# Performance work log

Measured on AMD Instinct MI355X. Metric: run time of the kernel, lower is better.

## Reference

```python
import jax, jax.numpy as jnp
import numpy as np

N, D, H = 4096, 4096, 8          # total tokens, model dim (=hidden), heads
DH = D // H                      # head dim = 512
NEG = jnp.float32(-1e9)


def _make_num_rels():
    rng = np.random.default_rng(0)
    lens = rng.integers(96, 161, size=31)
    last = N - int(lens.sum())
    assert last > 0
    return np.concatenate([lens, [last]]).astype(np.int64)


def setup_inputs() -> dict:
    key = jax.random.key(0)
    ks = jax.random.split(key, 9)
    s = 0.02
    inp = {
        "prod_rep": jax.random.normal(ks[0], (N, D), dtype=jnp.float32),
        "num_rels": jnp.asarray(_make_num_rels()),
        # torch Linear weights stored transposed: [in, out]
        "Wq": jax.random.normal(ks[1], (D, D), dtype=jnp.float32) * s,
        "bq": jnp.zeros((D,), dtype=jnp.float32),
        "Wk": jax.random.normal(ks[2], (D, D), dtype=jnp.float32) * s,
        "bk": jnp.zeros((D,), dtype=jnp.float32),
        "Wv": jax.random.normal(ks[3], (D, D), dtype=jnp.float32) * s,
        "bv": jnp.zeros((D,), dtype=jnp.float32),
        "Wfc": jax.random.normal(ks[4], (D, D), dtype=jnp.float32) * s,
        "bfc": jnp.zeros((D,), dtype=jnp.float32),
    }
    return inp


def reference(prod_rep, num_rels, Wq, bq, Wk, bk, Wv, bv, Wfc, bfc):
    n = prod_rep.shape[0]
    # segment id per token (tokens are laid out contiguously per segment)
    cum = jnp.cumsum(num_rels)
    seg = jnp.searchsorted(cum, jnp.arange(n), side="right")  # [N]

    # fused QKV projections over all tokens at once
    q = (prod_rep @ Wq + bq).reshape(n, H, DH)
    k = (prod_rep @ Wk + bk).reshape(n, H, DH)
    v = (prod_rep @ Wv + bv).reshape(n, H, DH)

    # block-diagonal attention: tokens only attend within their own segment
    scores = jnp.einsum("nhd,mhd->hnm", q, k) / jnp.sqrt(jnp.float32(DH))
    mask = seg[:, None] == seg[None, :]                        # [N, N]
    scores = jnp.where(mask[None, :, :], scores, NEG)
    probs = jax.nn.softmax(scores, axis=-1)                    # [H, N, N]
    context = jnp.einsum("hnm,mhd->nhd", probs, v).reshape(n, D)

    res1 = context + prod_rep
    res2 = res1 + (res1 @ Wfc + bfc)
    return res2
```

## Files before the change

kernel.cpp:

```cpp
#include <hip/hip_runtime.h>
#include <hip/hip_bf16.h>
#include <cstdint>

typedef __bf16 bf16;
typedef __attribute__((ext_vector_type(4))) __bf16 bf16x4;
typedef __attribute__((ext_vector_type(8))) __bf16 bf16x8;
typedef __attribute__((ext_vector_type(4))) float f32x4;

#define AS1 __attribute__((address_space(1)))
#define AS3 __attribute__((address_space(3)))

__device__ __forceinline__ unsigned short f2bf(float x) {
    union { __bf16 b; unsigned short u; } c;
    c.b = (__bf16)x;
    return c.u;
}

__device__ __forceinline__ void gld_lds16(const void* g, void* lds_wave_base) {
#if __has_builtin(__builtin_amdgcn_global_load_lds)
    __builtin_amdgcn_global_load_lds((AS1 void*)(uintptr_t)g,
                                     (AS3 void*)(uint32_t)(uintptr_t)lds_wave_base,
                                     16u, 0, 0u);
#else
    int lane = threadIdx.x & 63;
    *(uint4*)((char*)lds_wave_base + lane * 16) = *(const uint4*)g;
#endif
}

__global__ __launch_bounds__(256) void cvt_kernel(const float* __restrict__ in,
                                                  bf16* __restrict__ out) {
    int i = (blockIdx.x * 256 + threadIdx.x) * 4;
    float4 v = *(const float4*)&in[i];
    bf16x4 o;
    o[0] = (__bf16)v.x; o[1] = (__bf16)v.y; o[2] = (__bf16)v.z; o[3] = (__bf16)v.w;
    *(bf16x4*)&out[i] = o;
}

__global__ __launch_bounds__(256) void cvt_transpose_kernel(const float* __restrict__ in,
                                                            unsigned short* __restrict__ out, int n) {
    __shared__ unsigned short tile[64][65];
    int t = threadIdx.x;
    int n0 = blockIdx.x * 64, k0 = blockIdx.y * 64;
#pragma unroll
    for (int i = 0; i < 4; i++) {
        int idx = t + i * 256;
        int r = idx >> 4, cc = (idx & 15) * 4;
        float4 v = *(const float4*)&in[(size_t)(k0 + r) * n + n0 + cc];
        tile[r][cc + 0] = f2bf(v.x); tile[r][cc + 1] = f2bf(v.y);
        tile[r][cc + 2] = f2bf(v.z); tile[r][cc + 3] = f2bf(v.w);
    }
    __syncthreads();
#pragma unroll
    for (int i = 0; i < 4; i++) {
        int idx = t + i * 256;
        int nn = idx >> 4, kc = (idx & 15) * 4;
        ushort4 v;
        v.x = tile[kc + 0][nn]; v.y = tile[kc + 1][nn];
        v.z = tile[kc + 2][nn]; v.w = tile[kc + 3][nn];
        *(ushort4*)&out[(size_t)(n0 + nn) * n + k0 + kc] = v;
    }
}

__global__ __launch_bounds__(256) void transpose_bf16_kernel(const unsigned short* __restrict__ in,
                                                             unsigned short* __restrict__ out, int n) {
    __shared__ unsigned short tile[64][65];
    int t = threadIdx.x;
    int n0 = blockIdx.x * 64, k0 = blockIdx.y * 64;
#pragma unroll
    for (int i = 0; i < 4; i++) {
        int idx = t + i * 256;
        int r = idx >> 4, cc = (idx & 15) * 4;
        ushort4 v = *(const ushort4*)&in[(size_t)(k0 + r) * n + n0 + cc];
        tile[r][cc + 0] = v.x; tile[r][cc + 1] = v.y;
        tile[r][cc + 2] = v.z; tile[r][cc + 3] = v.w;
    }
    __syncthreads();
#pragma unroll
    for (int i = 0; i < 4; i++) {
        int idx = t + i * 256;
        int nn = idx >> 4, kc = (idx & 15) * 4;
        ushort4 v;
        v.x = tile[kc + 0][nn]; v.y = tile[kc + 1][nn];
        v.z = tile[kc + 2][nn]; v.w = tile[kc + 3][nn];
        *(ushort4*)&out[(size_t)(n0 + nn) * n + k0 + kc] = v;
    }
}


__device__ __forceinline__ void stage_khalf(const bf16* __restrict__ gb, int ldk, int kcol0,
                                            bf16* dst ) {
    const int t = threadIdx.x;
    const int wave = t >> 6;
#pragma unroll
    for (int i = 0; i < 2; i++) {
        int idx = i * 512 + t;
        int line = idx >> 3;
        int slot = (idx & 7) ^ (line & 7);
        int row = line * 2 + (slot >> 2);
        int kc = (slot & 3) * 8;
        gld_lds16(gb + (size_t)row * ldk + kcol0 + kc,
                  dst + (size_t)(i * 512 + wave * 64) * 8);
    }
}

__device__ __forceinline__ bf16x8 frag_ld(const bf16* sub, int r, int lq) {
    int line = r >> 1;
    int slot = (((r & 1) << 2) | lq) ^ (line & 7);
    return *(const bf16x8*)((const char*)sub + line * 128 + slot * 16);
}

template <int MODE>
__global__ __launch_bounds__(512, 2) void gemm256_kernel(
    const bf16* __restrict__ A, const bf16* __restrict__ BT,
    const float* __restrict__ bias, const bf16* __restrict__ resid,
    void* __restrict__ Cout, int M, int N, int K) {
    __shared__ __align__(16) bf16 lds[65536];
    const int tid = threadIdx.x;
    const int wave = tid >> 6, lane = tid & 63;
    const int lq = lane >> 4, lm = lane & 15;
    const int wr = wave >> 2, wcq = wave & 3;

    const int nwg = gridDim.x;
    const int chunk = nwg >> 3;
    const int bid = blockIdx.x;
    const int swz = (bid & 7) * chunk + (bid >> 3);
    const unsigned nbn = (unsigned)(N >> 8);
    const int bm = (int)((unsigned)swz / nbn);
    const int bn = (int)((unsigned)swz % nbn);
    const int row0 = bm << 8, col0 = bn << 8;

    const bf16* Ag = A + (size_t)row0 * K;
    const bf16* Bg = BT + (size_t)col0 * K;
    bf16* buf0 = lds;
    bf16* buf1 = lds + 32768;
    const int nT = K >> 6;

    f32x4 acc[8][4];
#pragma unroll
    for (int i = 0; i < 8; i++)
#pragma unroll
        for (int j = 0; j < 4; j++) acc[i][j] = (f32x4){0.f, 0.f, 0.f, 0.f};

    stage_khalf(Ag, K, 0, buf0);
    stage_khalf(Bg, K, 0, buf0 + 16384);
    stage_khalf(Ag, K, 32, buf0 + 8192);
    stage_khalf(Bg, K, 32, buf0 + 24576);
    stage_khalf(Ag, K, 64, buf1);
    stage_khalf(Bg, K, 64, buf1 + 16384);
    asm volatile("s_waitcnt vmcnt(4)" ::: "memory");
    __builtin_amdgcn_s_barrier();

    const int arow = wr * 128 + lm;
    const int brow = wcq * 64 + lm;

    bf16x8 a0[4], a1[4], b0[4], b1[4];
#pragma unroll
    for (int i = 0; i < 4; i++) a0[i] = frag_ld(buf0, arow + i * 16, lq);
#pragma unroll
    for (int j = 0; j < 4; j++) b0[j] = frag_ld(buf0 + 16384, brow + j * 16, lq);

    for (int t = 0; t < nT; ++t) {
        bf16* X = (t & 1) ? buf1 : buf0;
        bf16* Y = (t & 1) ? buf0 : buf1;
        const bf16* XA0 = X;
        const bf16* XA1 = X + 8192;
        const bf16* XB1 = X + 24576;
        const int kc1 = (t + 1) << 6;
        const int kc2 = (t + 2) << 6;

#pragma unroll
        for (int i = 0; i < 4; i++) a1[i] = frag_ld(XA0, arow + 64 + i * 16, lq);
        if (t + 1 < nT) stage_khalf(Ag, K, kc1 + 32, Y + 8192);
        __builtin_amdgcn_s_setprio(1);
#pragma unroll
        for (int i = 0; i < 4; i++)
#pragma unroll
            for (int j = 0; j < 4; j++)
                acc[i][j] = __builtin_amdgcn_mfma_f32_16x16x32_bf16(a0[i], b0[j], acc[i][j], 0, 0, 0);
        __builtin_amdgcn_s_setprio(0);

        asm volatile("s_waitcnt lgkmcnt(0)" ::: "memory");
        __builtin_amdgcn_s_barrier();
#pragma unroll
        for (int i = 0; i < 4; i++) a0[i] = frag_ld(XA1, arow + i * 16, lq);
#pragma unroll
        for (int j = 0; j < 4; j++) b1[j] = frag_ld(XB1, brow + j * 16, lq);
        if (t + 1 < nT) stage_khalf(Bg, K, kc1 + 32, Y + 24576);
        __builtin_amdgcn_s_setprio(1);
#pragma unroll
        for (int i = 0; i < 4; i++)
#pragma unroll
            for (int j = 0; j < 4; j++)
                acc[4 + i][j] = __builtin_amdgcn_mfma_f32_16x16x32_bf16(a1[i], b0[j], acc[4 + i][j], 0, 0, 0);
        __builtin_amdgcn_s_setprio(0);

#pragma unroll
        for (int i = 0; i < 4; i++) a1[i] = frag_ld(XA1, arow + 64 + i * 16, lq);
        if (t + 2 < nT) stage_khalf(Ag, K, kc2, X);
        __builtin_amdgcn_s_setprio(1);
#pragma unroll
        for (int i = 0; i < 4; i++)
#pragma unroll
            for (int j = 0; j < 4; j++)
                acc[i][j] = __builtin_amdgcn_mfma_f32_16x16x32_bf16(a0[i], b1[j], acc[i][j], 0, 0, 0);
        __builtin_amdgcn_s_setprio(0);

        asm volatile("s_waitcnt lgkmcnt(0)" ::: "memory");
        if (t + 2 < nT) stage_khalf(Bg, K, kc2, X + 16384);
        if (t < nT - 2) {
            asm volatile("s_waitcnt vmcnt(4)" ::: "memory");
        } else {
            asm volatile("s_waitcnt vmcnt(0)" ::: "memory");
        }
        __builtin_amdgcn_s_barrier();
        if (t + 1 < nT) {
#pragma unroll
            for (int i = 0; i < 4; i++) a0[i] = frag_ld(Y, arow + i * 16, lq);
#pragma unroll
            for (int j = 0; j < 4; j++) b0[j] = frag_ld(Y + 16384, brow + j * 16, lq);
        }
        __builtin_amdgcn_s_setprio(1);
#pragma unroll
        for (int i = 0; i < 4; i++)
#pragma unroll
            for (int j = 0; j < 4; j++)
                acc[4 + i][j] = __builtin_amdgcn_mfma_f32_16x16x32_bf16(a1[i], b1[j], acc[4 + i][j], 0, 0, 0);
        __builtin_amdgcn_s_setprio(0);
    }

#pragma unroll
    for (int nt = 0; nt < 4; nt++) {
        int col = col0 + wcq * 64 + nt * 16 + lm;
        float bv = bias[col];
#pragma unroll
        for (int mt = 0; mt < 8; mt++) {
            int rbase = row0 + wr * 128 + mt * 16 + lq * 4;
#pragma unroll
            for (int r = 0; r < 4; r++) {
                int row = rbase + r;
                float v = acc[mt][nt][r] + bv;
                if (MODE == 0) {
                    ((bf16*)Cout)[(size_t)row * N + col] = (bf16)v;
                } else {
                    v += (float)resid[(size_t)row * N + col];
                    ((float*)Cout)[(size_t)row * N + col] = v;
                }
            }
        }
    }
}

__global__ __launch_bounds__(256, 2) void attn_kernel(
    const bf16* __restrict__ Q, const bf16* __restrict__ K, const bf16* __restrict__ Vt,
    const int* __restrict__ num_rels, const float* __restrict__ X,
    bf16* __restrict__ R1) {
    const float SCALE = 0.044194173824159216f;
    int seg = blockIdx.x >> 3;
    int h = blockIdx.x & 7;
    int S = 0;
    for (int i = 0; i < seg; i++) S += num_rels[i];
    int L = num_rels[seg];
    int i0 = blockIdx.y * 64;
    if (i0 >= L) return;

    __shared__ __align__(16) bf16 Ks[32][520];
    __shared__ __align__(16) bf16 Vs[512][40];
    __shared__ __align__(16) bf16 Ps[4][16][40];

    const int t = threadIdx.x;
    const int wave = t >> 6, lane = t & 63;
    const int lq = lane >> 4, lm = lane & 15;

    const int qrow = i0 + wave * 16 + lm;
    const bool qvalid = qrow < L;
    bf16x8 aq[16];
    {
        const bf16* qb = Q + (size_t)(S + qrow) * 4096 + h * 512 + lq * 8;
#pragma unroll
        for (int c = 0; c < 16; c++) {
            bf16x8 v = {};
            if (qvalid) v = *(const bf16x8*)(qb + c * 32);
            aq[c] = v;
        }
    }

    f32x4 accO[32];
#pragma unroll
    for (int i = 0; i < 32; i++) accO[i] = (f32x4){0.f, 0.f, 0.f, 0.f};
    float m_r[4], l_r[4];
#pragma unroll
    for (int r = 0; r < 4; r++) { m_r[r] = -1e30f; l_r[r] = 0.f; }

    for (int j0 = 0; j0 < L; j0 += 32) {
#pragma unroll
        for (int it = 0; it < 8; it++) {
            int c = t + it * 256;
            int r = c >> 6, cc = (c & 63) * 8;
            *(uint4*)&Ks[r][cc] = *(const uint4*)&K[(size_t)(S + j0 + r) * 4096 + h * 512 + cc];
        }
#pragma unroll
        for (int it = 0; it < 8; it++) {
            int c = t + it * 256;
            int r = c >> 2, cc = (c & 3) * 8;
            *(uint4*)&Vs[r][cc] = *(const uint4*)&Vt[(size_t)(h * 512 + r) * 4096 + S + j0 + cc];
        }
        __syncthreads();

        f32x4 accS[2];
        accS[0] = (f32x4){0.f, 0.f, 0.f, 0.f};
        accS[1] = (f32x4){0.f, 0.f, 0.f, 0.f};
#pragma unroll
        for (int ct = 0; ct < 2; ct++)
#pragma unroll
            for (int c = 0; c < 16; c++) {
                bf16x8 bk = *(const bf16x8*)&Ks[ct * 16 + lm][c * 32 + lq * 8];
                accS[ct] = __builtin_amdgcn_mfma_f32_16x16x32_bf16(aq[c], bk, accS[ct], 0, 0, 0);
            }

        bool v0 = (j0 + lm) < L, v1 = (j0 + 16 + lm) < L;
        float p0v[4], p1v[4], alpha[4];
#pragma unroll
        for (int r = 0; r < 4; r++) {
            float s0 = v0 ? accS[0][r] * SCALE : -1e30f;
            float s1 = v1 ? accS[1][r] * SCALE : -1e30f;
            float mx = fmaxf(s0, s1);
#pragma unroll
            for (int o = 1; o < 16; o <<= 1) mx = fmaxf(mx, __shfl_xor(mx, o, 64));
            float mnew = fmaxf(m_r[r], mx);
            alpha[r] = __expf(m_r[r] - mnew);
            float p0 = __expf(s0 - mnew), p1 = __expf(s1 - mnew);
            float sum = p0 + p1;
#pragma unroll
            for (int o = 1; o < 16; o <<= 1) sum += __shfl_xor(sum, o, 64);
            l_r[r] = l_r[r] * alpha[r] + sum;
            m_r[r] = mnew;
            p0v[r] = p0; p1v[r] = p1;
        }
#pragma unroll
        for (int r = 0; r < 4; r++) {
            Ps[wave][lq * 4 + r][lm] = (bf16)p0v[r];
            Ps[wave][lq * 4 + r][16 + lm] = (bf16)p1v[r];
        }
#pragma unroll
        for (int i = 0; i < 32; i++)
#pragma unroll
            for (int r = 0; r < 4; r++) accO[i][r] *= alpha[r];

        bf16x8 ap = *(const bf16x8*)&Ps[wave][lm][lq * 8];
#pragma unroll
        for (int ct2 = 0; ct2 < 32; ct2++) {
            bf16x8 bv = *(const bf16x8*)&Vs[ct2 * 16 + lm][lq * 8];
            accO[ct2] = __builtin_amdgcn_mfma_f32_16x16x32_bf16(ap, bv, accO[ct2], 0, 0, 0);
        }
        __syncthreads();
    }

#pragma unroll
    for (int r = 0; r < 4; r++) {
        int row = i0 + wave * 16 + lq * 4 + r;
        if (row >= L) continue;
        float inv = 1.f / l_r[r];
        size_t base = (size_t)(S + row) * 4096 + h * 512;
#pragma unroll
        for (int ct2 = 0; ct2 < 32; ct2++) {
            int col = ct2 * 16 + lm;
            R1[base + col] = (bf16)(accO[ct2][r] * inv + X[base + col]);
        }
    }
}

extern "C" void kernel_launch(void* const* d_in, const int* in_sizes, int n_in,
                              void* d_out, int out_size, void* d_ws, size_t ws_size,
                              hipStream_t stream) {
    const float* prod = (const float*)d_in[0];
    const int* nr = (const int*)d_in[1];
    const float* Wq = (const float*)d_in[2];
    const float* bq = (const float*)d_in[3];
    const float* Wk = (const float*)d_in[4];
    const float* bk = (const float*)d_in[5];
    const float* Wv = (const float*)d_in[6];
    const float* bv = (const float*)d_in[7];
    const float* Wfc = (const float*)d_in[8];
    const float* bfc = (const float*)d_in[9];
    float* out = (float*)d_out;

    const size_t MATB = (size_t)4096 * 4096 * sizeof(bf16);
    char* ws = (char*)d_ws;
    bf16* Xb = (bf16*)(ws + 0 * MATB);
    bf16* Qb = (bf16*)(ws + 1 * MATB);
    bf16* Kb = (bf16*)(ws + 2 * MATB);
    bf16* Vb = (bf16*)(ws + 3 * MATB);
    bf16* WT = (bf16*)(ws + 4 * MATB);

    int nseg = in_sizes[1];

    dim3 cb(256), cg(16384);
    dim3 tb(256), tg(64, 64);
    dim3 gb(512), gg(256);

    cvt_kernel<<<cg, cb, 0, stream>>>(prod, Xb);

    cvt_transpose_kernel<<<tg, tb, 0, stream>>>(Wq, (unsigned short*)WT, 4096);
    gemm256_kernel<0><<<gg, gb, 0, stream>>>(Xb, WT, bq, nullptr, Qb, 4096, 4096, 4096);
    cvt_transpose_kernel<<<tg, tb, 0, stream>>>(Wk, (unsigned short*)WT, 4096);
    gemm256_kernel<0><<<gg, gb, 0, stream>>>(Xb, WT, bk, nullptr, Kb, 4096, 4096, 4096);
    cvt_transpose_kernel<<<tg, tb, 0, stream>>>(Wv, (unsigned short*)WT, 4096);
    gemm256_kernel<0><<<gg, gb, 0, stream>>>(Xb, WT, bv, nullptr, Vb, 4096, 4096, 4096);

    transpose_bf16_kernel<<<tg, tb, 0, stream>>>((const unsigned short*)Vb, (unsigned short*)Xb, 4096);

    dim3 ab(256), ag(nseg * 8, 18);
    attn_kernel<<<ag, ab, 0, stream>>>(Qb, Kb, Xb, nr, prod, Qb);

    cvt_transpose_kernel<<<tg, tb, 0, stream>>>(Wfc, (unsigned short*)WT, 4096);
    gemm256_kernel<1><<<gg, gb, 0, stream>>>(Qb, WT, bfc, Qb, out, 4096, 4096, 4096);
}
```

Baseline: 939.9 us.

## Use five-slot LDS ring buffer in GEMM to drop mid-iteration barrier

```diff
diff --git a/kernel.cpp b/kernel.cpp
--- a/kernel.cpp
+++ b/kernel.cpp
@@ -114,7 +114,7 @@
     const bf16* __restrict__ A, const bf16* __restrict__ BT,
     const float* __restrict__ bias, const bf16* __restrict__ resid,
     void* __restrict__ Cout, int M, int N, int K) {
-    __shared__ __align__(16) bf16 lds[65536];
+    __shared__ __align__(16) bf16 lds[81920];
     const int tid = threadIdx.x;
     const int wave = tid >> 6, lane = tid & 63;
     const int lq = lane >> 4, lm = lane & 15;
@@ -131,22 +131,23 @@
 
     const bf16* Ag = A + (size_t)row0 * K;
     const bf16* Bg = BT + (size_t)col0 * K;
-    bf16* buf0 = lds;
-    bf16* buf1 = lds + 32768;
     const int nT = K >> 6;
 
+#define SUBA(h) (lds + (size_t)((h) % 5) * 8192)
+#define SUBB(h) (lds + 40960 + (size_t)((h) % 5) * 8192)
+
     f32x4 acc[8][4];
 #pragma unroll
     for (int i = 0; i < 8; i++)
 #pragma unroll
         for (int j = 0; j < 4; j++) acc[i][j] = (f32x4){0.f, 0.f, 0.f, 0.f};
 
-    stage_khalf(Ag, K, 0, buf0);
-    stage_khalf(Bg, K, 0, buf0 + 16384);
-    stage_khalf(Ag, K, 32, buf0 + 8192);
-    stage_khalf(Bg, K, 32, buf0 + 24576);
-    stage_khalf(Ag, K, 64, buf1);
-    stage_khalf(Bg, K, 64, buf1 + 16384);
+    stage_khalf(Ag, K, 0, SUBA(0));
+    stage_khalf(Bg, K, 0, SUBB(0));
+    stage_khalf(Ag, K, 32, SUBA(1));
+    stage_khalf(Bg, K, 32, SUBB(1));
+    stage_khalf(Ag, K, 64, SUBA(2));
+    stage_khalf(Bg, K, 64, SUBB(2));
     asm volatile("s_waitcnt vmcnt(4)" ::: "memory");
     __builtin_amdgcn_s_barrier();
 
@@ -155,22 +156,18 @@
 
     bf16x8 a0[4], a1[4], b0[4], b1[4];
 #pragma unroll
-    for (int i = 0; i < 4; i++) a0[i] = frag_ld(buf0, arow + i * 16, lq);
-#pragma unroll
-    for (int j = 0; j < 4; j++) b0[j] = frag_ld(buf0 + 16384, brow + j * 16, lq);
+    for (int i = 0; i < 4; i++) a0[i] = frag_ld(SUBA(0), arow + i * 16, lq);
+#pragma unroll
+    for (int j = 0; j < 4; j++) b0[j] = frag_ld(SUBB(0), brow + j * 16, lq);
 
     for (int t = 0; t < nT; ++t) {
-        bf16* X = (t & 1) ? buf1 : buf0;
-        bf16* Y = (t & 1) ? buf0 : buf1;
-        const bf16* XA0 = X;
-        const bf16* XA1 = X + 8192;
-        const bf16* XB1 = X + 24576;
-        const int kc1 = (t + 1) << 6;
-        const int kc2 = (t + 2) << 6;
-
-#pragma unroll
-        for (int i = 0; i < 4; i++) a1[i] = frag_ld(XA0, arow + 64 + i * 16, lq);
-        if (t + 1 < nT) stage_khalf(Ag, K, kc1 + 32, Y + 8192);
+        const bf16* Ak0 = SUBA(2 * t);
+        const bf16* Ak1 = SUBA(2 * t + 1);
+        const bf16* Bk1 = SUBB(2 * t + 1);
+
+#pragma unroll
+        for (int i = 0; i < 4; i++) a1[i] = frag_ld(Ak0, arow + 64 + i * 16, lq);
+        if (t < nT - 1) stage_khalf(Ag, K, (2 * t + 3) * 32, SUBA(2 * t + 3));
         __builtin_amdgcn_s_setprio(1);
 #pragma unroll
         for (int i = 0; i < 4; i++)
@@ -179,13 +176,11 @@
                 acc[i][j] = __builtin_amdgcn_mfma_f32_16x16x32_bf16(a0[i], b0[j], acc[i][j], 0, 0, 0);
         __builtin_amdgcn_s_setprio(0);
 
-        asm volatile("s_waitcnt lgkmcnt(0)" ::: "memory");
-        __builtin_amdgcn_s_barrier();
-#pragma unroll
-        for (int i = 0; i < 4; i++) a0[i] = frag_ld(XA1, arow + i * 16, lq);
-#pragma unroll
-        for (int j = 0; j < 4; j++) b1[j] = frag_ld(XB1, brow + j * 16, lq);
-        if (t + 1 < nT) stage_khalf(Bg, K, kc1 + 32, Y + 24576);
+#pragma unroll
+        for (int i = 0; i < 4; i++) a0[i] = frag_ld(Ak1, arow + i * 16, lq);
+#pragma unroll
+        for (int j = 0; j < 4; j++) b1[j] = frag_ld(Bk1, brow + j * 16, lq);
+        if (t < nT - 1) stage_khalf(Bg, K, (2 * t + 3) * 32, SUBB(2 * t + 3));
         __builtin_amdgcn_s_setprio(1);
 #pragma unroll
         for (int i = 0; i < 4; i++)
@@ -195,8 +190,8 @@
         __builtin_amdgcn_s_setprio(0);
 
 #pragma unroll
-        for (int i = 0; i < 4; i++) a1[i] = frag_ld(XA1, arow + 64 + i * 16, lq);
-        if (t + 2 < nT) stage_khalf(Ag, K, kc2, X);
+        for (int i = 0; i < 4; i++) a1[i] = frag_ld(Ak1, arow + 64 + i * 16, lq);
+        if (t < nT - 2) stage_khalf(Ag, K, (2 * t + 4) * 32, SUBA(2 * t + 4));
         __builtin_amdgcn_s_setprio(1);
 #pragma unroll
         for (int i = 0; i < 4; i++)
@@ -205,8 +200,8 @@
                 acc[i][j] = __builtin_amdgcn_mfma_f32_16x16x32_bf16(a0[i], b1[j], acc[i][j], 0, 0, 0);
         __builtin_amdgcn_s_setprio(0);
 
+        if (t < nT - 2) stage_khalf(Bg, K, (2 * t + 4) * 32, SUBB(2 * t + 4));
         asm volatile("s_waitcnt lgkmcnt(0)" ::: "memory");
-        if (t + 2 < nT) stage_khalf(Bg, K, kc2, X + 16384);
         if (t < nT - 2) {
             asm volatile("s_waitcnt vmcnt(4)" ::: "memory");
         } else {
@@ -214,10 +209,12 @@
         }
         __builtin_amdgcn_s_barrier();
         if (t + 1 < nT) {
-#pragma unroll
-            for (int i = 0; i < 4; i++) a0[i] = frag_ld(Y, arow + i * 16, lq);
-#pragma unroll
-            for (int j = 0; j < 4; j++) b0[j] = frag_ld(Y + 16384, brow + j * 16, lq);
+            const bf16* An = SUBA(2 * t + 2);
+            const bf16* Bn = SUBB(2 * t + 2);
+#pragma unroll
+            for (int i = 0; i < 4; i++) a0[i] = frag_ld(An, arow + i * 16, lq);
+#pragma unroll
+            for (int j = 0; j < 4; j++) b0[j] = frag_ld(Bn, brow + j * 16, lq);
         }
         __builtin_amdgcn_s_setprio(1);
 #pragma unroll
@@ -227,6 +224,8 @@
                 acc[4 + i][j] = __builtin_amdgcn_mfma_f32_16x16x32_bf16(a1[i], b1[j], acc[4 + i][j], 0, 0, 0);
         __builtin_amdgcn_s_setprio(0);
     }
+#undef SUBA
+#undef SUBB
 
 #pragma unroll
     for (int nt = 0; nt < 4; nt++) {
```

Measured after the change: 947.9 us. About the same (+0.9%).
